# Kernel optimization log

Hardware: AMD Instinct MI355X
Metric: run time of the kernel (lower is better)

## Reference

```python
import jax, jax.numpy as jnp
import numpy as np

RADIUS = 6
KSIZE = 2 * RADIUS + 1  # 13


def setup_inputs() -> dict:
    key = jax.random.key(0)
    k1, k2 = jax.random.split(key)
    B, C, H, W = 8, 256, 128, 128
    z_t = jax.random.normal(k1, (B, C, H, W), dtype=jnp.float32)
    z_t1 = jax.random.normal(k2, (B, C, H, W), dtype=jnp.float32)
    return {"z_t": z_t, "z_t1": z_t1}


def reference(z_t, z_t1):
    B, C, H, W = z_t.shape
    r, K = RADIUS, KSIZE
    # zero-pad neighbor frame spatially (matches F.unfold padding=radius)
    zp = jnp.pad(z_t1, ((0, 0), (0, 0), (r, r), (r, r)))
    # kernel tap offsets in torch-unfold order: index k = i*K + j (row-major)
    ii, jj = jnp.meshgrid(jnp.arange(K), jnp.arange(K), indexing="ij")
    offsets = jnp.stack([ii.reshape(-1), jj.reshape(-1)], axis=-1)  # [K*K, 2]

    def tap(carry, off):
        # window: padded[:, :, i:i+H, j:j+W]  == z_t1 shifted by (i-r, j-r)
        win = jax.lax.dynamic_slice(zp, (0, 0, off[0], off[1]), (B, C, H, W))
        s = jnp.einsum("bchw,bchw->bhw", z_t, win)  # channel dot per pixel
        return carry, s

    _, scores = jax.lax.scan(tap, None, offsets)  # [K*K, B, H, W]
    scores = jnp.transpose(scores, (1, 0, 2, 3))  # [B, K*K, H, W]
    return scores / jnp.sqrt(jnp.asarray(C, dtype=z_t.dtype))
```

## Files before the change

kernel.cpp:

```cpp
#include <hip/hip_runtime.h>
#include <hip/hip_bf16.h>


#define CHPL 16384
#define NT 169
#define KHALF 85
#define OSTRIDE 132
#define BFRAG 35840
#define AFRAG_OFF (2*BFRAG)
#define SMTOT (AFRAG_OFF + 8192)

typedef __attribute__((ext_vector_type(8))) short bf16x8;
typedef __attribute__((ext_vector_type(4))) float f32x4;
typedef unsigned int u32;
typedef unsigned short u16;

static __device__ __forceinline__ u32 pk2(float a, float b) {
    __hip_bfloat162 h = __float22bfloat162_rn(make_float2(a, b));
    union { __hip_bfloat162 h2; u32 u; } c; c.h2 = h; return c.u;
}

__global__ __launch_bounds__(256)
void lc_tr(const float* __restrict__ zt1, void* __restrict__ ws) {
    __shared__ float ld[64][68];
    const int tid = threadIdx.x, bid = blockIdx.x;
    const int cb = bid & 3, wb = (bid >> 2) & 1;
    const int h = (bid >> 3) & 127, b = bid >> 10;
    if (bid == 0 && tid < 128) ((u32*)ws)[tid] = 0u;
    const int c0 = cb * 64, w0 = wb * 64;
#pragma unroll
    for (int k = 0; k < 4; ++k) {
        const int u = tid + k * 256, ch = u >> 4, seg = u & 15;
        const float4 v = *(const float4*)(zt1 + ((size_t)(b * 256 + c0 + ch)) * CHPL
                                          + h * 128 + w0 + seg * 4);
        *(float4*)&ld[ch][seg * 4] = v;
    }
    __syncthreads();
    const int px = tid >> 2, part = tid & 3;
    u32 r[8];
#pragma unroll
    for (int j = 0; j < 8; ++j)
        r[j] = pk2(ld[part * 16 + 2 * j][px], ld[part * 16 + 2 * j + 1][px]);
    u16* dst = (u16*)((char*)ws + 512)
               + ((size_t)(b * 16384 + h * 128 + w0 + px)) * 256 + c0 + part * 16;
    *(uint4*)dst = make_uint4(r[0], r[1], r[2], r[3]);
    *(uint4*)(dst + 8) = make_uint4(r[4], r[5], r[6], r[7]);
}

__global__ __launch_bounds__(512, 4)
void lc9(const float* __restrict__ zt, const void* __restrict__ ws,
         float* __restrict__ out) {
    __shared__ union { char raw[SMTOT]; float outb[KHALF * OSTRIDE]; } sm;
    char* smb = sm.raw;
    const int tid = threadIdx.x, lane = tid & 63, wid = tid >> 6;
    const int bid = blockIdx.x;
    const int b = bid & 7, t = bid >> 3;
    const int h0 = (t >> 3) * 8, w0 = (t & 7) * 16;
    const int py0 = (wid >> 2) * 4, px0 = (wid & 3) * 4;
    const int nlo = lane & 3, nhi = (lane >> 2) & 3, oo = lane >> 4;

    const u16* zw = (const u16*)((const char*)ws + 512);
    const char* zpg = (const char*)ws;

    const char* bsrc[5]; int badv[5]; int bdst[5];
    if (wid < 7) {
#pragma unroll
        for (int i = 0; i < 5; ++i) {
            const int I = wid * 5 + i;
            const int g = I * 64 + lane;
            const int px = g >> 2, slot = g & 3;
            const int qy = px / 28, qx = px % 28;
            const int gy = h0 + qy - 6, gx = w0 + qx - 6;
            const bool val = (gy >= 0) && (gy < 128) && (gx >= 0) && (gx < 128);
            const int ss = slot ^ ((px >> 1) & 3);
            bsrc[i] = val ? (const char*)(zw + ((size_t)(b * 16384 + gy * 128 + gx)) * 256
                                          + ss * 8)
                          : zpg;
            badv[i] = val ? 64 : 0;
            bdst[i] = I * 1024;
        }
    }

#define BISSUE(PAR) if (wid < 7) { _Pragma("unroll")                           \
    for (int i = 0; i < 5; ++i) {                                              \
        __builtin_amdgcn_global_load_lds(                                      \
            (const __attribute__((address_space(1))) void*)bsrc[i],            \
            (__attribute__((address_space(3))) void*)(smb + (PAR)*BFRAG + bdst[i]), \
            16, 0, 0);                                                         \
        bsrc[i] += badv[i]; } }

    const int octA = tid >> 7, pxu = tid & 127;
    const float* asrc = zt + ((size_t)(b * 256 + octA * 8)) * CHPL
                        + (h0 + (pxu >> 4)) * 128 + w0 + (pxu & 15);
    const int awoff = AFRAG_OFF + pxu * 64 + ((octA ^ ((pxu >> 1) & 3)) << 4);
    float pfA[2][8];

#define AISSUE(KC, PAR) { _Pragma("unroll")                                    \
    for (int e = 0; e < 8; ++e)                                                \
        pfA[PAR][e] = asrc[((size_t)((KC) * 32 + e)) * CHPL]; }

#define APACK(PAR) { uint4 q;                                                  \
    q.x = pk2(pfA[PAR][0], pfA[PAR][1]); q.y = pk2(pfA[PAR][2], pfA[PAR][3]);  \
    q.z = pk2(pfA[PAR][4], pfA[PAR][5]); q.w = pk2(pfA[PAR][6], pfA[PAR][7]);  \
    *(uint4*)(smb + awoff) = q; }

    int boff[16];
#pragma unroll
    for (int qi = 0; qi < 16; ++qi) {
        const int px = (py0 + (qi >> 2) * 4 + nhi) * 28 + (px0 + (qi & 3) * 4 + nlo);
        boff[qi] = px * 64 + ((oo ^ ((px >> 1) & 3)) << 4);
    }
    const int pxm = (py0 + nhi) * 16 + px0 + nlo;
    const int aoff = AFRAG_OFF + pxm * 64 + ((oo ^ ((pxm >> 1) & 3)) << 4);

    f32x4 acc[16];
#pragma unroll
    for (int qi = 0; qi < 16; ++qi) acc[qi] = (f32x4){0.f, 0.f, 0.f, 0.f};

    BISSUE(0) AISSUE(0, 0)
#pragma unroll
    for (int kc = 0; kc < 8; ++kc) {
        asm volatile("s_waitcnt vmcnt(0)\n\ts_barrier" ::: "memory");
        if (kc < 7) { BISSUE((kc + 1) & 1) AISSUE(kc + 1, (kc + 1) & 1) }
        APACK(kc & 1)
        asm volatile("s_waitcnt lgkmcnt(0)\n\ts_barrier" ::: "memory");
        const char* fb = smb + (kc & 1) * BFRAG;
        const bf16x8 af = *(const bf16x8*)(smb + aoff);
#pragma unroll
        for (int qi = 0; qi < 16; ++qi) {
            const bf16x8 bfr = *(const bf16x8*)(fb + boff[qi]);
            acc[qi] = __builtin_amdgcn_mfma_f32_16x16x32_bf16(af, bfr, acc[qi], 0, 0, 0);
        }
    }
    __syncthreads();

    const int psb = (py0 + oo) * 16 + px0;
#pragma unroll 1
    for (int pass = 0; pass < 2; ++pass) {
        const int kb = pass * KHALF;
        const int nk = pass ? (NT - KHALF) : KHALF;
#pragma unroll
        for (int qi = 0; qi < 16; ++qi) {
            const int di = 4 * (qi >> 2) + nhi - oo;
            const bool diok = (unsigned)di <= 12u;
            const int dib = di * 13;
#pragma unroll
            for (int r = 0; r < 4; ++r) {
                const int dj = 4 * (qi & 3) + nlo - r;
                const int k  = dib + dj;
                if (diok && (unsigned)dj <= 12u && k >= kb && k < kb + nk)
                    sm.outb[(k - kb) * OSTRIDE + psb + r] = acc[qi][r] * 0.0625f;
            }
        }
        __syncthreads();
        const int total4 = nk * 32;
        for (int i = tid; i < total4; i += 512) {
            const int row = i >> 5, j = i & 31;
            const float4 val = *(const float4*)&sm.outb[row * OSTRIDE + j * 4];
            float* dst = out + (((size_t)(b * NT + kb + row) * 128 + h0 + (j >> 2)) * 128
                                + w0 + (j & 3) * 4);
            *(float4*)dst = val;
        }
        __syncthreads();
    }
}

extern "C" void kernel_launch(void* const* d_in, const int* in_sizes, int n_in,
                              void* d_out, int out_size, void* d_ws, size_t ws_size,
                              hipStream_t stream) {
    const float* zt  = (const float*)d_in[0];
    const float* zt1 = (const float*)d_in[1];
    float* out = (float*)d_out;
    lc_tr<<<dim3(8192), dim3(256), 0, stream>>>(zt1, d_ws);
    lc9<<<dim3(1024), dim3(512), 0, stream>>>(zt, d_ws, out);
}
```

Before: 148.3 us.

## Load MFMA operands directly from global memory into registers, dropping LDS staging

Replaces the double-buffered LDS staging of the bf16 neighbor halo (global_load_lds) and the A-fragment pack-through-LDS with direct per-lane global loads into registers. All eight A chunks are preloaded and converted up front, and each B fragment is read straight from the transposed workspace. The zero page grows to 4 KB so out-of-bounds lanes read zeros without a guard. This removes the per-chunk barriers and LDS traffic and shrinks shared memory to the output staging buffer, which allows more occupancy. The cost is redundant global/L2 reads, since each halo pixel is fetched by many waves instead of once per block, and more register pressure.

```diff
diff --git a/kernel.cpp b/kernel.cpp
--- a/kernel.cpp
+++ b/kernel.cpp
@@ -6,9 +6,7 @@
 #define NT 169
 #define KHALF 85
 #define OSTRIDE 132
-#define BFRAG 35840
-#define AFRAG_OFF (2*BFRAG)
-#define SMTOT (AFRAG_OFF + 8192)
+#define ZPG 4096
 
 typedef __attribute__((ext_vector_type(8))) short bf16x8;
 typedef __attribute__((ext_vector_type(4))) float f32x4;
@@ -26,7 +24,7 @@
     const int tid = threadIdx.x, bid = blockIdx.x;
     const int cb = bid & 3, wb = (bid >> 2) & 1;
     const int h = (bid >> 3) & 127, b = bid >> 10;
-    if (bid == 0 && tid < 128) ((u32*)ws)[tid] = 0u;
+    if (bid == 0) ((uint4*)ws)[tid] = make_uint4(0u, 0u, 0u, 0u);
     const int c0 = cb * 64, w0 = wb * 64;
 #pragma unroll
     for (int k = 0; k < 4; ++k) {
@@ -41,17 +39,16 @@
 #pragma unroll
     for (int j = 0; j < 8; ++j)
         r[j] = pk2(ld[part * 16 + 2 * j][px], ld[part * 16 + 2 * j + 1][px]);
-    u16* dst = (u16*)((char*)ws + 512)
+    u16* dst = (u16*)((char*)ws + ZPG)
                + ((size_t)(b * 16384 + h * 128 + w0 + px)) * 256 + c0 + part * 16;
     *(uint4*)dst = make_uint4(r[0], r[1], r[2], r[3]);
     *(uint4*)(dst + 8) = make_uint4(r[4], r[5], r[6], r[7]);
 }
 
-__global__ __launch_bounds__(512, 4)
-void lc9(const float* __restrict__ zt, const void* __restrict__ ws,
-         float* __restrict__ out) {
-    __shared__ union { char raw[SMTOT]; float outb[KHALF * OSTRIDE]; } sm;
-    char* smb = sm.raw;
+__global__ __launch_bounds__(512)
+void lc10(const float* __restrict__ zt, const void* __restrict__ ws,
+          float* __restrict__ out) {
+    __shared__ union { char raw[KHALF * OSTRIDE * 4]; float outb[KHALF * OSTRIDE]; } sm;
     const int tid = threadIdx.x, lane = tid & 63, wid = tid >> 6;
     const int bid = blockIdx.x;
     const int b = bid & 7, t = bid >> 3;
@@ -59,86 +56,55 @@
     const int py0 = (wid >> 2) * 4, px0 = (wid & 3) * 4;
     const int nlo = lane & 3, nhi = (lane >> 2) & 3, oo = lane >> 4;
 
-    const u16* zw = (const u16*)((const char*)ws + 512);
-    const char* zpg = (const char*)ws;
+    const char* wsb = (const char*)ws;
 
-    const char* bsrc[5]; int badv[5]; int bdst[5];
-    if (wid < 7) {
+    u32 off[16];
 #pragma unroll
-        for (int i = 0; i < 5; ++i) {
-            const int I = wid * 5 + i;
-            const int g = I * 64 + lane;
-            const int px = g >> 2, slot = g & 3;
-            const int qy = px / 28, qx = px % 28;
-            const int gy = h0 + qy - 6, gx = w0 + qx - 6;
-            const bool val = (gy >= 0) && (gy < 128) && (gx >= 0) && (gx < 128);
-            const int ss = slot ^ ((px >> 1) & 3);
-            bsrc[i] = val ? (const char*)(zw + ((size_t)(b * 16384 + gy * 128 + gx)) * 256
-                                          + ss * 8)
-                          : zpg;
-            badv[i] = val ? 64 : 0;
-            bdst[i] = I * 1024;
+    for (int qi = 0; qi < 16; ++qi) {
+        const int qyL = py0 + (qi >> 2) * 4 + nhi;
+        const int qxL = px0 + (qi & 3) * 4 + nlo;
+        const int gy = h0 + qyL - 6, gx = w0 + qxL - 6;
+        const bool val = (gy >= 0) && (gy < 128) && (gx >= 0) && (gx < 128);
+        off[qi] = val ? (u32)(ZPG + ((size_t)(b * 16384 + gy * 128 + gx)) * 512
+                              + oo * 16)
+                      : (u32)(lane * 16);
+    }
+
+    bf16x8 abf[8];
+    {
+        const float* ap = zt + (((size_t)(b * 256 + oo * 8)) * CHPL
+                                + (h0 + py0 + nhi) * 128 + (w0 + px0 + nlo));
+#pragma unroll
+        for (int pr = 0; pr < 8; ++pr) {
+            float a8[8];
+#pragma unroll
+            for (int e = 0; e < 8; ++e) a8[e] = ap[(size_t)(pr * 32 + e) * CHPL];
+            union { u32 u[4]; bf16x8 v; } au;
+            au.u[0] = pk2(a8[0], a8[1]); au.u[1] = pk2(a8[2], a8[3]);
+            au.u[2] = pk2(a8[4], a8[5]); au.u[3] = pk2(a8[6], a8[7]);
+            abf[pr] = au.v;
         }
     }
-
-#define BISSUE(PAR) if (wid < 7) { _Pragma("unroll")                           \
-    for (int i = 0; i < 5; ++i) {                                              \
-        __builtin_amdgcn_global_load_lds(                                      \
-            (const __attribute__((address_space(1))) void*)bsrc[i],            \
-            (__attribute__((address_space(3))) void*)(smb + (PAR)*BFRAG + bdst[i]), \
-            16, 0, 0);                                                         \
-        bsrc[i] += badv[i]; } }
-
-    const int octA = tid >> 7, pxu = tid & 127;
-    const float* asrc = zt + ((size_t)(b * 256 + octA * 8)) * CHPL
-                        + (h0 + (pxu >> 4)) * 128 + w0 + (pxu & 15);
-    const int awoff = AFRAG_OFF + pxu * 64 + ((octA ^ ((pxu >> 1) & 3)) << 4);
-    float pfA[2][8];
-
-#define AISSUE(KC, PAR) { _Pragma("unroll")                                    \
-    for (int e = 0; e < 8; ++e)                                                \
-        pfA[PAR][e] = asrc[((size_t)((KC) * 32 + e)) * CHPL]; }
-
-#define APACK(PAR) { uint4 q;                                                  \
-    q.x = pk2(pfA[PAR][0], pfA[PAR][1]); q.y = pk2(pfA[PAR][2], pfA[PAR][3]);  \
-    q.z = pk2(pfA[PAR][4], pfA[PAR][5]); q.w = pk2(pfA[PAR][6], pfA[PAR][7]);  \
-    *(uint4*)(smb + awoff) = q; }
-
-    int boff[16];
-#pragma unroll
-    for (int qi = 0; qi < 16; ++qi) {
-        const int px = (py0 + (qi >> 2) * 4 + nhi) * 28 + (px0 + (qi & 3) * 4 + nlo);
-        boff[qi] = px * 64 + ((oo ^ ((px >> 1) & 3)) << 4);
-    }
-    const int pxm = (py0 + nhi) * 16 + px0 + nlo;
-    const int aoff = AFRAG_OFF + pxm * 64 + ((oo ^ ((pxm >> 1) & 3)) << 4);
 
     f32x4 acc[16];
 #pragma unroll
     for (int qi = 0; qi < 16; ++qi) acc[qi] = (f32x4){0.f, 0.f, 0.f, 0.f};
 
-    BISSUE(0) AISSUE(0, 0)
 #pragma unroll
     for (int kc = 0; kc < 8; ++kc) {
-        asm volatile("s_waitcnt vmcnt(0)\n\ts_barrier" ::: "memory");
-        if (kc < 7) { BISSUE((kc + 1) & 1) AISSUE(kc + 1, (kc + 1) & 1) }
-        APACK(kc & 1)
-        asm volatile("s_waitcnt lgkmcnt(0)\n\ts_barrier" ::: "memory");
-        const char* fb = smb + (kc & 1) * BFRAG;
-        const bf16x8 af = *(const bf16x8*)(smb + aoff);
 #pragma unroll
         for (int qi = 0; qi < 16; ++qi) {
-            const bf16x8 bfr = *(const bf16x8*)(fb + boff[qi]);
-            acc[qi] = __builtin_amdgcn_mfma_f32_16x16x32_bf16(af, bfr, acc[qi], 0, 0, 0);
+            const bf16x8 bfr = *(const bf16x8*)(wsb + off[qi] + kc * 64);
+            acc[qi] = __builtin_amdgcn_mfma_f32_16x16x32_bf16(abf[kc], bfr, acc[qi], 0, 0, 0);
         }
     }
-    __syncthreads();
 
     const int psb = (py0 + oo) * 16 + px0;
 #pragma unroll 1
     for (int pass = 0; pass < 2; ++pass) {
         const int kb = pass * KHALF;
         const int nk = pass ? (NT - KHALF) : KHALF;
+        __syncthreads();
 #pragma unroll
         for (int qi = 0; qi < 16; ++qi) {
             const int di = 4 * (qi >> 2) + nhi - oo;
@@ -161,7 +127,6 @@
                                 + w0 + (j & 3) * 4);
             *(float4*)dst = val;
         }
-        __syncthreads();
     }
 }
 
@@ -172,5 +137,5 @@
     const float* zt1 = (const float*)d_in[1];
     float* out = (float*)d_out;
     lc_tr<<<dim3(8192), dim3(256), 0, stream>>>(zt1, d_ws);
-    lc9<<<dim3(1024), dim3(512), 0, stream>>>(zt, d_ws, out);
+    lc10<<<dim3(1024), dim3(512), 0, stream>>>(zt, d_ws, out);
 }
```

Result: slower. 212.1 us (+43.0%).
